# Performance work log

Hardware: AMD Instinct MI355X
Metric: run time of the kernel (lower is better)

## Reference

```python
import jax, jax.numpy as jnp
import numpy as np

MARGIN = 70.0
THR = 125.0
PD_EPS = 1e-6  # torch F.pairwise_distance default eps


def _return_cam(features, weight_softmax, class_idx):
    # features: [bz, nc, h, w]; weight_softmax: [n_cls, nc]; class_idx: [bz]
    w_sel = weight_softmax[class_idx]                     # [bz, nc]
    cam = jnp.einsum('bc,bchw->bhw', w_sel, features)     # [bz, h, w]
    cam = cam - cam.min(axis=(1, 2), keepdims=True)
    cam = cam / cam.max(axis=(1, 2), keepdims=True) * 255.0
    return cam[:, None]                                   # [bz, 1, h, w]


def _pairwise_distance(x, y):
    # torch F.pairwise_distance: ||x - y + eps||_2 along last dim
    return jnp.sqrt(jnp.sum((x - y + PD_EPS) ** 2, axis=-1))


def setup_inputs() -> dict:
    key = jax.random.key(0)
    ks = jax.random.split(key, 6)
    bz, nc, h, w, n_cls = 64, 2048, 14, 14, 1000
    return {
        'pred': jax.random.normal(ks[0], (bz, n_cls), jnp.float32),
        'cla_truth': jax.random.randint(ks[1], (bz,), 0, n_cls, jnp.int32),
        'seg_truth': jax.random.uniform(ks[2], (bz, h, w), jnp.float32),
        'features_blobs': jax.random.normal(ks[3], (bz, nc, h, w), jnp.float32),
        'weight_softmax': jax.random.normal(ks[4], (n_cls, nc), jnp.float32),
        'idx': jax.random.randint(ks[5], (bz, 3), 0, n_cls, jnp.int32),
    }


def reference(pred, cla_truth, seg_truth, features_blobs, weight_softmax, idx):
    bz, nc, h, w = features_blobs.shape
    # cross entropy
    logp = jax.nn.log_softmax(pred, axis=-1)
    loss1 = -jnp.mean(logp[jnp.arange(bz), cla_truth])
    # CAMs for top-3 predicted classes
    cam0 = _return_cam(features_blobs, weight_softmax, idx[:, 0])  # [bz,1,h,w]
    cam1 = _return_cam(features_blobs, weight_softmax, idx[:, 1])
    cam2 = _return_cam(features_blobs, weight_softmax, idx[:, 2])
    # binarize cam0 (values in [0,255]); <=thr -> 0, >thr -> 1
    dst = jnp.where(cam0[:, 0] > THR, 1.0, 0.0)                     # [bz,h,w]
    # row-wise distance to seg truth, averaged over rows
    ed1 = jnp.mean(_pairwise_distance(dst, seg_truth), axis=1)      # [bz]
    # CAM-weighted features via broadcasted matmul (requires h == w)
    fea0 = jnp.matmul(cam0, features_blobs)                         # [bz,nc,h,w]
    fea1 = jnp.matmul(cam1, features_blobs)
    fea2 = jnp.matmul(cam2, features_blobs)
    d01 = _pairwise_distance(fea0.reshape(bz, -1), fea1.reshape(bz, -1)) / nc
    d02 = _pairwise_distance(fea0.reshape(bz, -1), fea2.reshape(bz, -1)) / nc
    loss_dis = jnp.mean(ed1 + jnp.clip(MARGIN - d01 - d02, 0.0, None)) + loss1
    return loss_dis
```

## Files before the change

kernel.cpp:

```cpp
#include <hip/hip_runtime.h>
#include <hip/hip_bf16.h>
#include <math.h>

#define BZ      64
#define NC      2048
#define HH      14
#define HW      196
#define NCLS    1000
#define SPLITS  8
#define CPB     (NC/SPLITS)
#define CHN     16
#define NCHUNK  (CPB/CHN)
#define NCT     224

#define CAM_OFF  0
#define G_OFF    (BZ*SPLITS*3*HW)
#define S_OFF    (G_OFF + BZ*SPLITS*HW)
#define TERM_OFF (S_OFF + BZ*SPLITS*HH)

__global__ __launch_bounds__(256) void k_stage1(
    const float* __restrict__ F, const float* __restrict__ W,
    const int* __restrict__ idx, float* __restrict__ ws)
{
  __shared__ __align__(16) float Fs[2][CHN*HW];
  __shared__ __align__(16) float wls[3][CPB];
  __shared__ __align__(16) float SC[35*225];
  __shared__ float SCB[224];

  const int t = threadIdx.x;
  const int s = blockIdx.x;
  const int b = blockIdx.y;
  const int cbase = s*CPB;

  const int i0 = idx[b*3+0], i1 = idx[b*3+1], i2 = idx[b*3+2];
  wls[0][t] = W[(size_t)i0*NC + cbase + t];
  wls[1][t] = W[(size_t)i1*NC + cbase + t];
  wls[2][t] = W[(size_t)i2*NC + cbase + t];

  const float* Fb = F + ((size_t)b*NC + cbase)*HW;

  const bool isC = (t < NCT);
  const int cg = t / 14;
  const int jj = t % 14;

  float gacc[105];
  float cam0[14], cam1[14], cam2[14], sacc[14];
  #pragma unroll
  for (int e=0;e<105;e++) gacc[e]=0.f;
  #pragma unroll
  for (int m=0;m<14;m++){ cam0[m]=0.f; cam1[m]=0.f; cam2[m]=0.f; sacc[m]=0.f; }

  float4 pre0, pre1, pre2, pre3;
  auto loadChunk = [&](int ch){
    const float4* src = (const float4*)Fb + (size_t)ch*784;
    pre0 = src[t]; pre1 = src[t+256]; pre2 = src[t+512];
    if (t < 16) pre3 = src[t+768];
  };
  auto storeChunk = [&](int bufi){
    float4* dst = (float4*)&Fs[bufi][0];
    dst[t]=pre0; dst[t+256]=pre1; dst[t+512]=pre2;
    if (t < 16) dst[t+768]=pre3;
  };

  loadChunk(0);
  storeChunk(0);
  __syncthreads();

  for (int ch = 0; ch < NCHUNK; ++ch){
    const int bufi = ch & 1;
    if (ch+1 < NCHUNK) loadChunk(ch+1);

    if (isC){
      const float w0 = wls[0][ch*CHN + cg];
      const float w1 = wls[1][ch*CHN + cg];
      const float w2 = wls[2][ch*CHN + cg];
      const float* base = &Fs[bufi][cg*HW + jj];
      float v[14];
      #pragma unroll
      for (int m=0;m<14;m++) v[m] = base[m*14];
      #pragma unroll
      for (int m=0;m<14;m++){
        sacc[m] += v[m];
        cam0[m] += w0*v[m];
        cam1[m] += w1*v[m];
        cam2[m] += w2*v[m];
      }
      int e=0;
      #pragma unroll
      for (int m=0;m<14;m++){
        #pragma unroll
        for (int mp=m;mp<14;mp++){ gacc[e] += v[m]*v[mp]; e++; }
      }
    }

    if (ch+1 < NCHUNK) storeChunk((ch+1)&1);
    __syncthreads();
  }

  const size_t pslot = (size_t)(b*SPLITS + s);

  #pragma unroll
  for (int r=0;r<3;r++){
    if (isC){
      #pragma unroll
      for (int el=0; el<35; el++) SC[el*225 + t] = gacc[r*35 + el];
    }
    __syncthreads();
    if (t < 210){
      const int el = t / 6, g = t % 6;
      const int start = g*38, len = (g==5)? 34 : 38;
      float a = 0.f;
      for (int i=0;i<len;i++) a += SC[el*225 + start + i];
      SCB[el*6 + g] = a;
    }
    __syncthreads();
    if (t < 35){
      float a = 0.f;
      #pragma unroll
      for (int g=0; g<6; g++) a += SCB[t*6 + g];
      int e = r*35 + t, m = 0, rem = e;
      while (rem >= 14 - m){ rem -= 14 - m; m++; }
      int mp = m + rem;
      float* gb = ws + G_OFF + pslot*HW;
      gb[m*HH + mp] = a;
      if (mp > m) gb[mp*HH + m] = a;
    }
    __syncthreads();
  }

  #pragma unroll
  for (int k=0;k<3;k++){
    if (isC){
      #pragma unroll
      for (int m=0;m<14;m++)
        SC[(m*14 + jj)*17 + cg] = (k==0)? cam0[m] : (k==1)? cam1[m] : cam2[m];
    }
    __syncthreads();
    if (t < HW){
      float a = 0.f;
      #pragma unroll
      for (int i=0;i<16;i++) a += SC[t*17 + i];
      ws[CAM_OFF + pslot*3*HW + k*HW + t] = a;
    }
    __syncthreads();
  }

  if (isC){
    #pragma unroll
    for (int m=0;m<14;m++) SC[m*225 + t] = sacc[m];
  }
  __syncthreads();
  if (t < NCT){
    const int m = t % 14, g = t / 14;
    float a = 0.f;
    #pragma unroll
    for (int i=0;i<14;i++) a += SC[m*225 + g*14 + i];
    SCB[m*16 + g] = a;
  }
  __syncthreads();
  if (t < HH){
    float a = 0.f;
    #pragma unroll
    for (int g=0; g<16; g++) a += SCB[t*16 + g];
    ws[S_OFF + pslot*HH + t] = a;
  }
}

template<int MODE>
__device__ __forceinline__ float bred(float v, float* red){
  #pragma unroll
  for (int o=32;o>0;o>>=1){
    float u = __shfl_down(v, o, 64);
    if (MODE==0) v += u; else if (MODE==1) v = fminf(v,u); else v = fmaxf(v,u);
  }
  __syncthreads();
  if ((threadIdx.x & 63)==0) red[threadIdx.x>>6] = v;
  __syncthreads();
  float r = red[0];
  #pragma unroll
  for (int w=1;w<4;w++){
    float u = red[w];
    if (MODE==0) r += u; else if (MODE==1) r = fminf(r,u); else r = fmaxf(r,u);
  }
  return r;
}

__global__ __launch_bounds__(256) void k_stage2(
    const float* __restrict__ pred, const int* __restrict__ cla,
    const float* __restrict__ seg, float* __restrict__ ws)
{
  const int t = threadIdx.x, b = blockIdx.x;
  __shared__ float cam[3][HW], Gm[HW], Sv[HH];
  __shared__ float D1[HW], D2[HW], EE[HW];
  __shared__ float rowv[HH], dc1[HH], dc2[HH];
  __shared__ float red[4];
  __shared__ float scal[6];

  if (t < HW){
    for (int k=0;k<3;k++){
      float a=0.f;
      for (int s=0;s<SPLITS;s++)
        a += ws[CAM_OFF + ((size_t)(b*SPLITS+s)*3 + k)*HW + t];
      cam[k][t]=a;
    }
    float g=0.f;
    for (int s=0;s<SPLITS;s++) g += ws[G_OFF + (size_t)(b*SPLITS+s)*HW + t];
    Gm[t]=g;
  }
  if (t < HH){
    float a=0.f;
    for (int s=0;s<SPLITS;s++) a += ws[S_OFF + (size_t)(b*SPLITS+s)*HH + t];
    Sv[t]=a;
  }
  __syncthreads();

  for (int k=0;k<3;k++){
    float v = (t<HW)? cam[k][t] : 3.0e38f;
    float mn = bred<1>(v, red);
    v = (t<HW)? cam[k][t] : -3.0e38f;
    float mx = bred<2>(v, red);
    if (t==0){ scal[2*k]=mn; scal[2*k+1]=mx; }
  }
  __syncthreads();

  if (t < HW){
    float c0 = (cam[0][t]-scal[0]) / (scal[1]-scal[0]) * 255.0f;
    float c1 = (cam[1][t]-scal[2]) / (scal[3]-scal[2]) * 255.0f;
    float c2 = (cam[2][t]-scal[4]) / (scal[5]-scal[4]) * 255.0f;
    float dst = (c0 > 125.0f) ? 1.0f : 0.0f;
    D1[t] = c0 - c1; D2[t] = c0 - c2;
    float e = dst - seg[(size_t)b*HW + t] + 1e-6f;
    EE[t] = e*e;
  }
  __syncthreads();

  if (t < HH){
    float rs=0.f, d1=0.f, d2=0.f;
    #pragma unroll
    for (int j=0;j<HH;j++){
      rs += EE[t*HH+j];
      d1 += D1[j*HH+t];
      d2 += D2[j*HH+t];
    }
    rowv[t] = sqrtf(rs); dc1[t]=d1; dc2[t]=d2;
  }
  __syncthreads();

  float v1=0.f, v2=0.f;
  if (t < HW){
    int m = t/HH, mp = t%HH;
    float h1=0.f, h2=0.f;
    #pragma unroll
    for (int i=0;i<HH;i++){
      h1 += D1[i*HH+m]*D1[i*HH+mp];
      h2 += D2[i*HH+m]*D2[i*HH+mp];
    }
    v1 = h1*Gm[t]; v2 = h2*Gm[t];
  }
  float sx2_1 = bred<0>(v1, red);
  float sx2_2 = bred<0>(v2, red);

  const float* pb = pred + (size_t)b*NCLS;
  float mv = -3.0e38f;
  for (int i=t;i<NCLS;i+=256) mv = fmaxf(mv, pb[i]);
  mv = bred<2>(mv, red);
  float es = 0.f;
  for (int i=t;i<NCLS;i+=256) es += expf(pb[i]-mv);
  es = bred<0>(es, red);

  if (t==0){
    float lse = mv + logf(es);
    float ce  = lse - pb[cla[b]];
    float ed1 = 0.f;
    #pragma unroll
    for (int i=0;i<HH;i++) ed1 += rowv[i];
    ed1 *= (1.0f/14.0f);
    float sx1=0.f, sx2=0.f;
    #pragma unroll
    for (int m=0;m<HH;m++){ sx1 += dc1[m]*Sv[m]; sx2 += dc2[m]*Sv[m]; }
    const float NEPS2 = 401408.0f * 1e-12f;
    float d01 = sqrtf(sx2_1 + 2e-6f*sx1 + NEPS2) * (1.0f/2048.0f);
    float d02 = sqrtf(sx2_2 + 2e-6f*sx2 + NEPS2) * (1.0f/2048.0f);
    float term = ed1 + fmaxf(0.0f, 70.0f - d01 - d02) + ce;
    ws[TERM_OFF + b] = term;
  }
}

__global__ void k_stage3(const float* __restrict__ ws, float* __restrict__ out){
  float v = ws[TERM_OFF + threadIdx.x];
  #pragma unroll
  for (int o=32;o>0;o>>=1) v += __shfl_down(v, o, 64);
  if (threadIdx.x==0) out[0] = v * (1.0f/64.0f);
}

extern "C" void kernel_launch(void* const* d_in, const int* in_sizes, int n_in,
                              void* d_out, int out_size, void* d_ws, size_t ws_size,
                              hipStream_t stream) {
  const float* pred = (const float*)d_in[0];
  const int*   cla  = (const int*)  d_in[1];
  const float* seg  = (const float*)d_in[2];
  const float* F    = (const float*)d_in[3];
  const float* W    = (const float*)d_in[4];
  const int*   idx  = (const int*)  d_in[5];
  float* out = (float*)d_out;
  float* ws  = (float*)d_ws;

  dim3 g1(SPLITS, BZ);
  k_stage1<<<g1, 256, 0, stream>>>(F, W, idx, ws);
  k_stage2<<<BZ, 256, 0, stream>>>(pred, cla, seg, ws);
  k_stage3<<<1, 64, 0, stream>>>(ws, out);
}
```

Before: 183.3 us.

## Stream feature chunks directly into LDS and alias shared buffers

The double-buffered feature-chunk prefetch now uses global_load_lds so data goes straight from global memory into LDS, instead of being staged through float4 registers and stored afterwards. The Fs, wls and reduction scratch arrays are merged into one aliased shared buffer, which shrinks the LDS footprint, and launch_bounds is set to request two blocks per CU. The aim is to free the prefetch registers and the explicit LDS store instructions, and to allow more resident blocks. The change relies on the barrier waiting for the direct-to-LDS loads to complete. The scratch arrays also now overlap the feature buffers, so correctness depends on the reductions only running after the main loop.

```diff
diff --git a/kernel.cpp b/kernel.cpp
--- a/kernel.cpp
+++ b/kernel.cpp
@@ -18,14 +18,22 @@
 #define S_OFF    (G_OFF + BZ*SPLITS*HW)
 #define TERM_OFF (S_OFF + BZ*SPLITS*HH)
 
-__global__ __launch_bounds__(256) void k_stage1(
+__device__ __forceinline__ void gl_lds16(const float4* g, float* l){
+  __builtin_amdgcn_global_load_lds(
+      (const __attribute__((address_space(1))) void*)g,
+      (__attribute__((address_space(3))) void*)l, 16, 0, 0);
+}
+
+__global__ __launch_bounds__(256, 2) void k_stage1(
     const float* __restrict__ F, const float* __restrict__ W,
     const int* __restrict__ idx, float* __restrict__ ws)
 {
-  __shared__ __align__(16) float Fs[2][CHN*HW];
-  __shared__ __align__(16) float wls[3][CPB];
-  __shared__ __align__(16) float SC[35*225];
-  __shared__ float SCB[224];
+  __shared__ __align__(16) float U[8112];
+  float* const Fs0 = U;
+  float* const Fs1 = U + 3136;
+  float* const wls = U + 6272;
+  float* const SC  = U;
+  float* const SCB = U + 7875;
 
   const int t = threadIdx.x;
   const int s = blockIdx.x;
@@ -33,15 +41,17 @@
   const int cbase = s*CPB;
 
   const int i0 = idx[b*3+0], i1 = idx[b*3+1], i2 = idx[b*3+2];
-  wls[0][t] = W[(size_t)i0*NC + cbase + t];
-  wls[1][t] = W[(size_t)i1*NC + cbase + t];
-  wls[2][t] = W[(size_t)i2*NC + cbase + t];
+  wls[0*CPB + t] = W[(size_t)i0*NC + cbase + t];
+  wls[1*CPB + t] = W[(size_t)i1*NC + cbase + t];
+  wls[2*CPB + t] = W[(size_t)i2*NC + cbase + t];
 
   const float* Fb = F + ((size_t)b*NC + cbase)*HW;
+  const float4* Fb4 = (const float4*)Fb;
 
   const bool isC = (t < NCT);
   const int cg = t / 14;
   const int jj = t % 14;
+  const int wv = t >> 6;
 
   float gacc[105];
   float cam0[14], cam1[14], cam2[14], sacc[14];
@@ -50,31 +60,28 @@
   #pragma unroll
   for (int m=0;m<14;m++){ cam0[m]=0.f; cam1[m]=0.f; cam2[m]=0.f; sacc[m]=0.f; }
 
-  float4 pre0, pre1, pre2, pre3;
-  auto loadChunk = [&](int ch){
-    const float4* src = (const float4*)Fb + (size_t)ch*784;
-    pre0 = src[t]; pre1 = src[t+256]; pre2 = src[t+512];
-    if (t < 16) pre3 = src[t+768];
+  auto issue = [&](int ch, int bufi){
+    const float4* src = Fb4 + (size_t)ch*784;
+    float* dstBase = bufi ? Fs1 : Fs0;
+    #pragma unroll
+    for (int i=0;i<3;i++)
+      gl_lds16(src + i*256 + t, dstBase + (i*256 + wv*64)*4);
+    if (t < 16)
+      gl_lds16(src + 768 + t, dstBase + 768*4);
   };
-  auto storeChunk = [&](int bufi){
-    float4* dst = (float4*)&Fs[bufi][0];
-    dst[t]=pre0; dst[t+256]=pre1; dst[t+512]=pre2;
-    if (t < 16) dst[t+768]=pre3;
-  };
-
-  loadChunk(0);
-  storeChunk(0);
+
+  issue(0, 0);
   __syncthreads();
 
   for (int ch = 0; ch < NCHUNK; ++ch){
-    const int bufi = ch & 1;
-    if (ch+1 < NCHUNK) loadChunk(ch+1);
+    if (ch+1 < NCHUNK) issue(ch+1, (ch+1)&1);
 
     if (isC){
-      const float w0 = wls[0][ch*CHN + cg];
-      const float w1 = wls[1][ch*CHN + cg];
-      const float w2 = wls[2][ch*CHN + cg];
-      const float* base = &Fs[bufi][cg*HW + jj];
+      const float* Fsb = (ch & 1) ? Fs1 : Fs0;
+      const float w0 = wls[0*CPB + ch*CHN + cg];
+      const float w1 = wls[1*CPB + ch*CHN + cg];
+      const float w2 = wls[2*CPB + ch*CHN + cg];
+      const float* base = Fsb + cg*HW + jj;
       float v[14];
       #pragma unroll
       for (int m=0;m<14;m++) v[m] = base[m*14];
@@ -92,8 +99,6 @@
         for (int mp=m;mp<14;mp++){ gacc[e] += v[m]*v[mp]; e++; }
       }
     }
-
-    if (ch+1 < NCHUNK) storeChunk((ch+1)&1);
     __syncthreads();
   }
 
```

New measurement: 181.1 us. Within noise of the previous version (-1.2%).
